# Kernel optimization log

Measured on AMD Instinct MI355X. Metric: run time of the kernel, lower is better.

The kernel has to match this reference:

```python
import jax, jax.numpy as jnp
import numpy as np

N_NODES = 50000
N_RAND_EDGES = 500000
SELF_LOOP_W = 0.5  # fill_value in add_remaining_self_loops


def _build_graph(key):
    k1, k2, k3 = jax.random.split(key, 3)
    src = jax.random.randint(k1, (N_RAND_EDGES,), 0, N_NODES)
    dst = jax.random.randint(k2, (N_RAND_EDGES,), 0, N_NODES)
    # PPMI weights are positive log-ratios; simulate with positive uniforms
    w = jax.random.uniform(k3, (N_RAND_EDGES,), minval=0.1, maxval=2.0)
    loops = jnp.arange(N_NODES)
    row = jnp.concatenate([src, loops])
    col = jnp.concatenate([dst, loops])
    ew = jnp.concatenate([w, jnp.full((N_NODES,), SELF_LOOP_W, dtype=w.dtype)])
    # symmetric normalization: D^-1/2 A D^-1/2 (deg computed from row, as in norm())
    deg = jax.ops.segment_sum(ew, row, num_segments=N_NODES)
    dis = jnp.where(deg > 0, deg ** -0.5, 0.0)
    norm = (dis[row] * ew * dis[col]).astype(jnp.float32)
    edge_index = jnp.stack([row, col]).astype(jnp.int64)
    return edge_index, norm


def setup_inputs() -> dict:
    key = jax.random.key(0)
    kx, kg, kw1, kw2 = jax.random.split(key, 4)
    edge_index, norm = _build_graph(kg)
    feat, hid, emb = 256, 128, 64
    # glorot init
    s1 = np.sqrt(6.0 / (feat + hid))
    s2 = np.sqrt(6.0 / (hid + emb))
    return {
        "x": jax.random.normal(kx, (N_NODES, feat), dtype=jnp.float32),
        "edge_index": edge_index,
        "norm": norm,
        "W1": jax.random.uniform(kw1, (feat, hid), minval=-s1, maxval=s1, dtype=jnp.float32),
        "b1": jnp.zeros((hid,), dtype=jnp.float32),
        "W2": jax.random.uniform(kw2, (hid, emb), minval=-s2, maxval=s2, dtype=jnp.float32),
        "b2": jnp.zeros((emb,), dtype=jnp.float32),
    }


def _gcn_layer(x, row, col, norm, W, b):
    h = x @ W                                   # [N, out]
    msg = norm[:, None] * h[row]                # gather + scale per edge
    agg = jax.ops.segment_sum(msg, col, num_segments=N_NODES)  # scatter-add
    return agg + b


def reference(x, edge_index, norm, W1, b1, W2, b2):
    row, col = edge_index[0], edge_index[1]
    h = _gcn_layer(x, row, col, norm, W1, b1)
    h = jax.nn.relu(h)  # dropout is identity in eval
    return _gcn_layer(h, row, col, norm, W2, b2)
```

## Files before the change

kernel.cpp:

```cpp
#include <hip/hip_runtime.h>
#include <stdint.h>


typedef __attribute__((ext_vector_type(8))) short short8;
typedef __attribute__((ext_vector_type(4))) float f32x4;

#define SLOTS 48
#define OCAP  65536

__device__ __forceinline__ unsigned short f2bf(float f) {
    unsigned u = __float_as_uint(f);
    return (unsigned short)((u + 0x7FFFu + ((u >> 16) & 1u)) >> 16);
}
__device__ __forceinline__ float bf_lo(unsigned v) { return __uint_as_float(v << 16); }
__device__ __forceinline__ float bf_hi(unsigned v) { return __uint_as_float(v & 0xFFFF0000u); }
__device__ __forceinline__ float bf1(unsigned short v) { return __uint_as_float((unsigned)v << 16); }
__device__ __forceinline__ unsigned short f2h(float f) {
    _Float16 h = (_Float16)f;
    return __builtin_bit_cast(unsigned short, h);
}
__device__ __forceinline__ float h2f(unsigned u16) {
    _Float16 h = __builtin_bit_cast(_Float16, (unsigned short)(u16 & 0xFFFFu));
    return (float)h;
}

__global__ __launch_bounds__(256) void k_prep0(int* __restrict__ cursor, int n,
                                               int* __restrict__ ocount,
                                               const float* __restrict__ W1,
                                               const float* __restrict__ W2,
                                               unsigned short* __restrict__ W1t,
                                               unsigned short* __restrict__ W2t,
                                               int FEAT, int HID, int EMB) {
    const int gid = blockIdx.x * blockDim.x + threadIdx.x;
    const int stride = gridDim.x * blockDim.x;
    if (gid == 0) *ocount = 0;
    int4* c4 = (int4*)cursor;
    const int n4 = n >> 2;
    for (int j = gid; j < n4; j += stride) c4[j] = make_int4(0, 0, 0, 0);
    for (int j = (n4 << 2) + gid; j < n; j += stride) cursor[j] = 0;
    const int t1 = FEAT * HID, t2 = HID * EMB;
    for (int i = gid; i < t1 + t2; i += stride) {
        if (i < t1) {
            int k = i / HID, nn = i % HID;
            W1t[(size_t)nn * FEAT + k] = f2bf(W1[i]);
        } else {
            int j = i - t1;
            int k = j / EMB, nn = j % EMB;
            W2t[(size_t)nn * HID + k] = f2bf(W2[j]);
        }
    }
}

template <int BM, int BN, int FM, int FN, bool A_F32, bool OUT_BF16>
__device__ __forceinline__ void gemm_body(char* ldsA, char* ldsB,
                                          const void* __restrict__ Ag,
                                          const unsigned short* __restrict__ Bt,
                                          void* __restrict__ Cv,
                                          int M, int K, int N, int blk) {
    const int tid  = threadIdx.x;
    const int lane = tid & 63;
    const int wid  = tid >> 6;
    const int wr   = wid >> 1;
    const int wc   = wid & 1;
    const int m0   = blk * BM;

    f32x4 acc[FM][FN] = {};

    for (int k0 = 0; k0 < K; k0 += 64) {
        {
            const int row  = tid >> 2;
            const int kq   = tid & 3;
            const int grow = min(m0 + row, M - 1);
            const int kbb  = kq * 32;
            const int sw   = (row & 7) << 4;
            if (A_F32) {
                const float* src = (const float*)Ag + (size_t)grow * K + k0 + kq * 16;
                float4 v0 = ((const float4*)src)[0];
                float4 v1 = ((const float4*)src)[1];
                float4 v2 = ((const float4*)src)[2];
                float4 v3 = ((const float4*)src)[3];
                union { short8 s; unsigned short h[8]; } p0, p1;
                p0.h[0] = f2bf(v0.x); p0.h[1] = f2bf(v0.y);
                p0.h[2] = f2bf(v0.z); p0.h[3] = f2bf(v0.w);
                p0.h[4] = f2bf(v1.x); p0.h[5] = f2bf(v1.y);
                p0.h[6] = f2bf(v1.z); p0.h[7] = f2bf(v1.w);
                p1.h[0] = f2bf(v2.x); p1.h[1] = f2bf(v2.y);
                p1.h[2] = f2bf(v2.z); p1.h[3] = f2bf(v2.w);
                p1.h[4] = f2bf(v3.x); p1.h[5] = f2bf(v3.y);
                p1.h[6] = f2bf(v3.z); p1.h[7] = f2bf(v3.w);
                *(short8*)(ldsA + row * 128 + ( kbb       ^ sw)) = p0.s;
                *(short8*)(ldsA + row * 128 + ((kbb + 16) ^ sw)) = p1.s;
            } else {
                const unsigned short* src =
                    (const unsigned short*)Ag + (size_t)grow * K + k0 + kq * 16;
                short8 s0 = ((const short8*)src)[0];
                short8 s1 = ((const short8*)src)[1];
                *(short8*)(ldsA + row * 128 + ( kbb       ^ sw)) = s0;
                *(short8*)(ldsA + row * 128 + ((kbb + 16) ^ sw)) = s1;
            }
        }
        if (BN == 128 || tid < 128) {
            const int row = tid >> 1;
            const int kh  = tid & 1;
            const int sw  = (row & 7) << 4;
            const short8* src = (const short8*)(Bt + (size_t)row * K + k0 + kh * 32);
            #pragma unroll
            for (int j = 0; j < 4; ++j) {
                short8 s = src[j];
                int kb = kh * 64 + j * 16;
                *(short8*)(ldsB + row * 128 + (kb ^ sw)) = s;
            }
        }
        __syncthreads();

        #pragma unroll
        for (int s = 0; s < 2; ++s) {
            const int klo = s * 64 + (lane >> 4) * 16;
            short8 af[FM], bfv[FN];
            #pragma unroll
            for (int i = 0; i < FM; ++i) {
                int r = wr * (FM * 16) + i * 16 + (lane & 15);
                af[i] = *(const short8*)(ldsA + r * 128 + (klo ^ ((r & 7) << 4)));
            }
            #pragma unroll
            for (int j = 0; j < FN; ++j) {
                int n = wc * (FN * 16) + j * 16 + (lane & 15);
                bfv[j] = *(const short8*)(ldsB + n * 128 + (klo ^ ((n & 7) << 4)));
            }
            #pragma unroll
            for (int i = 0; i < FM; ++i)
                #pragma unroll
                for (int j = 0; j < FN; ++j)
                    acc[i][j] = __builtin_amdgcn_mfma_f32_16x16x32_bf16(
                        af[i], bfv[j], acc[i][j], 0, 0, 0);
        }
        __syncthreads();
    }

    #pragma unroll
    for (int i = 0; i < FM; ++i) {
        const int rbase = m0 + wr * (FM * 16) + i * 16 + ((lane >> 4) << 2);
        #pragma unroll
        for (int j = 0; j < FN; ++j) {
            const int c = wc * (FN * 16) + j * 16 + (lane & 15);
            #pragma unroll
            for (int r = 0; r < 4; ++r)
                if (rbase + r < M) {
                    if (OUT_BF16)
                        ((unsigned short*)Cv)[(size_t)(rbase + r) * N + c] = f2bf(acc[i][j][r]);
                    else
                        ((float*)Cv)[(size_t)(rbase + r) * N + c] = acc[i][j][r];
                }
        }
    }
}

template <int BM, int BN, int FM, int FN, bool A_F32, bool OUT_BF16>
__global__ __launch_bounds__(256) void k_gemm_mfma(const void* __restrict__ Ag,
                                                   const unsigned short* __restrict__ Bt,
                                                   void* __restrict__ Cv,
                                                   int M, int K, int N) {
    __shared__ char ldsA[BM * 128];
    __shared__ char ldsB[BN * 128];
    gemm_body<BM, BN, FM, FN, A_F32, OUT_BF16>(ldsA, ldsB, Ag, Bt, Cv, M, K, N,
                                               blockIdx.x);
}

template <int BM, int BN, int FM, int FN, bool A_F32, bool OUT_BF16>
__global__ __launch_bounds__(256) void k_gemm_scatter(const void* __restrict__ Ag,
                                                      const unsigned short* __restrict__ Bt,
                                                      void* __restrict__ Cv,
                                                      int M, int K, int N,
                                                      int gemmBlocks,
                                                      const int* __restrict__ ei,
                                                      const float* __restrict__ nrm,
                                                      int E, int Nn,
                                                      int* __restrict__ cursor,
                                                      unsigned* __restrict__ ent,
                                                      uint2* __restrict__ olist,
                                                      int* __restrict__ ocount) {
    __shared__ char ldsA[BM * 128];
    __shared__ char ldsB[BN * 128];
    if ((int)blockIdx.x < gemmBlocks) {
        gemm_body<BM, BN, FM, FN, A_F32, OUT_BF16>(ldsA, ldsB, Ag, Bt, Cv, M, K, N,
                                                   blockIdx.x);
        return;
    }
    __shared__ int sIs64;
    if (threadIdx.x < 64) {
        const int i = 1 + 2 * threadIdx.x;
        int z = (i < 2 * E) ? (ei[i] == 0) : 1;
        unsigned long long m = __ballot(z);
        if (threadIdx.x == 0) sIs64 = (m == ~0ULL) ? 1 : 0;
    }
    __syncthreads();
    const int is64 = sIs64;

    const int t  = (blockIdx.x - gemmBlocks) * blockDim.x + threadIdx.x;
    const int e0 = t * 4;
    if (e0 >= E) return;

    int r[4], c[4];
    float wv[4];
    int nv = 4;
    if (e0 + 3 < E) {
        if (is64) {
            const int4* pr = (const int4*)(ei + 2 * e0);
            const int4* pc = (const int4*)(ei + 2 * E + 2 * e0);
            int4 r01 = pr[0], r23 = pr[1], c01 = pc[0], c23 = pc[1];
            r[0] = r01.x; r[1] = r01.z; r[2] = r23.x; r[3] = r23.z;
            c[0] = c01.x; c[1] = c01.z; c[2] = c23.x; c[3] = c23.z;
        } else {
            int4 rr = *(const int4*)(ei + e0);
            int4 cc = *(const int4*)(ei + E + e0);
            r[0] = rr.x; r[1] = rr.y; r[2] = rr.z; r[3] = rr.w;
            c[0] = cc.x; c[1] = cc.y; c[2] = cc.z; c[3] = cc.w;
        }
        const float4 w4 = *(const float4*)(nrm + e0);
        wv[0] = w4.x; wv[1] = w4.y; wv[2] = w4.z; wv[3] = w4.w;
    } else {
        nv = E - e0;
        for (int i = 0; i < nv; ++i) {
            const int e = e0 + i;
            if (is64) { r[i] = ei[2 * e]; c[i] = ei[2 * (E + e)]; }
            else      { r[i] = ei[e];     c[i] = ei[E + e]; }
            wv[i] = nrm[e];
        }
    }
    #pragma unroll
    for (int i = 0; i < 4; ++i) {
        if (i < nv && (unsigned)c[i] < (unsigned)Nn && (unsigned)r[i] < (unsigned)Nn) {
            const unsigned entry = ((unsigned)r[i] << 16) | (unsigned)f2h(wv[i]);
            const int pos = atomicAdd(&cursor[c[i]], 1);
            if (pos < SLOTS) ent[(size_t)c[i] * SLOTS + pos] = entry;
            else { int op = atomicAdd(ocount, 1);
                   if (op < OCAP) olist[op] = make_uint2((unsigned)c[i], entry); }
        }
    }
}

template <int F, bool RELU, bool OUT_BF16>
__global__ __launch_bounds__(256) void k_agg(const unsigned short* __restrict__ h,
                                             const int* __restrict__ cursor,
                                             const unsigned* __restrict__ ent,
                                             const uint2* __restrict__ olist,
                                             const int* __restrict__ ocount,
                                             const float* __restrict__ bias,
                                             void* __restrict__ outp, int nnodes) {
    const int lane = threadIdx.x & 63;
    const int wid  = __builtin_amdgcn_readfirstlane(threadIdx.x >> 6);
    const int node = blockIdx.x * 4 + wid;
    if (node >= nnodes) return;
    const int deg = min(cursor[node], SLOTS);
    const unsigned* slots = ent + (size_t)node * SLOTS;
    const unsigned rmax = (unsigned)(nnodes - 1);

    if (F == 128) {
        const unsigned* hp = (const unsigned*)h;
        float2 a0 = {0.f, 0.f}, a1 = {0.f, 0.f}, a2 = {0.f, 0.f}, a3 = {0.f, 0.f};
        for (int g = 0; g < deg; g += 4) {
            uint4 q = *(const uint4*)(slots + g);
            const int rem = deg - g;
            float w0 = h2f(q.x), w1 = h2f(q.y), w2 = h2f(q.z), w3 = h2f(q.w);
            if (rem < 4) {
                w1 = (rem > 1) ? w1 : 0.f;
                w2 = (rem > 2) ? w2 : 0.f;
                w3 = 0.f;
                if (rem == 3) w3 = 0.f; else if (rem > 3) {}
            }
            const unsigned v0 = hp[(size_t)min(q.x >> 16, rmax) * 64 + lane];
            const unsigned v1 = hp[(size_t)min(q.y >> 16, rmax) * 64 + lane];
            const unsigned v2 = hp[(size_t)min(q.z >> 16, rmax) * 64 + lane];
            const unsigned v3 = hp[(size_t)min(q.w >> 16, rmax) * 64 + lane];
            a0.x = fmaf(w0, bf_lo(v0), a0.x); a0.y = fmaf(w0, bf_hi(v0), a0.y);
            a1.x = fmaf(w1, bf_lo(v1), a1.x); a1.y = fmaf(w1, bf_hi(v1), a1.y);
            a2.x = fmaf(w2, bf_lo(v2), a2.x); a2.y = fmaf(w2, bf_hi(v2), a2.y);
            a3.x = fmaf(w3, bf_lo(v3), a3.x); a3.y = fmaf(w3, bf_hi(v3), a3.y);
        }
        float2 acc;
        acc.x = (a0.x + a1.x) + (a2.x + a3.x);
        acc.y = (a0.y + a1.y) + (a2.y + a3.y);
        const int oc = *ocount;
        if (oc > 0) {
            for (int i = 0; i < oc && i < OCAP; ++i) {
                const uint2 it = olist[i];
                if ((int)it.x == node) {
                    const float w = h2f(it.y);
                    const unsigned v = hp[(size_t)min(it.y >> 16, rmax) * 64 + lane];
                    acc.x = fmaf(w, bf_lo(v), acc.x);
                    acc.y = fmaf(w, bf_hi(v), acc.y);
                }
            }
        }
        const float2 b = ((const float2*)bias)[lane];
        acc.x += b.x; acc.y += b.y;
        if (RELU) { acc.x = fmaxf(acc.x, 0.f); acc.y = fmaxf(acc.y, 0.f); }
        if (OUT_BF16) {
            unsigned pack = (unsigned)f2bf(acc.x) | ((unsigned)f2bf(acc.y) << 16);
            ((unsigned*)outp)[(size_t)node * 64 + lane] = pack;
        } else {
            ((float2*)outp)[(size_t)node * 64 + lane] = acc;
        }
    } else {
        float a0 = 0.f, a1 = 0.f, a2 = 0.f, a3 = 0.f;
        for (int g = 0; g < deg; g += 4) {
            uint4 q = *(const uint4*)(slots + g);
            const int rem = deg - g;
            float w0 = h2f(q.x), w1 = h2f(q.y), w2 = h2f(q.z), w3 = h2f(q.w);
            if (rem < 4) {
                w1 = (rem > 1) ? w1 : 0.f;
                w2 = (rem > 2) ? w2 : 0.f;
                w3 = 0.f;
            }
            const float f0 = bf1(h[(size_t)min(q.x >> 16, rmax) * 64 + lane]);
            const float f1 = bf1(h[(size_t)min(q.y >> 16, rmax) * 64 + lane]);
            const float f2 = bf1(h[(size_t)min(q.z >> 16, rmax) * 64 + lane]);
            const float f3 = bf1(h[(size_t)min(q.w >> 16, rmax) * 64 + lane]);
            a0 = fmaf(w0, f0, a0); a1 = fmaf(w1, f1, a1);
            a2 = fmaf(w2, f2, a2); a3 = fmaf(w3, f3, a3);
        }
        float acc = (a0 + a1) + (a2 + a3);
        const int oc = *ocount;
        if (oc > 0) {
            for (int i = 0; i < oc && i < OCAP; ++i) {
                const uint2 it = olist[i];
                if ((int)it.x == node)
                    acc = fmaf(h2f(it.y),
                               bf1(h[(size_t)min(it.y >> 16, rmax) * 64 + lane]), acc);
            }
        }
        acc += bias[lane];
        if (RELU) acc = fmaxf(acc, 0.f);
        ((float*)outp)[(size_t)node * 64 + lane] = acc;
    }
}


extern "C" void kernel_launch(void* const* d_in, const int* in_sizes, int n_in,
                              void* d_out, int out_size, void* d_ws, size_t ws_size,
                              hipStream_t stream) {
    const float* x   = (const float*)d_in[0];
    const int*   ei  = (const int*)d_in[1];
    const float* nrm = (const float*)d_in[2];
    const float* W1  = (const float*)d_in[3];
    const float* b1  = (const float*)d_in[4];
    const float* W2  = (const float*)d_in[5];
    const float* b2  = (const float*)d_in[6];
    float* out = (float*)d_out;

    const int HID  = in_sizes[4];
    const int FEAT = in_sizes[3] / HID;
    const int EMB  = in_sizes[5] / HID;
    const int Nn   = in_sizes[0] / FEAT;
    const int E    = in_sizes[2];
    const int entWords = Nn * SLOTS;

    char* p = (char*)d_ws;
    auto alloc = [&](size_t bytes) {
        char* r = p;
        p += (bytes + 255) & ~(size_t)255;
        return r;
    };
    unsigned short* h1b    = (unsigned short*)alloc((size_t)Nn * HID * 2);
    unsigned short* a1b    = (unsigned short*)alloc((size_t)Nn * HID * 2);
    unsigned short* h2b    = (unsigned short*)alloc((size_t)Nn * EMB * 2);
    unsigned short* W1t    = (unsigned short*)alloc((size_t)HID * FEAT * 2);
    unsigned short* W2t    = (unsigned short*)alloc((size_t)EMB * HID * 2);
    int*            cursor = (int*)           alloc((size_t)Nn * 4);
    unsigned*       ent    = (unsigned*)      alloc((size_t)entWords * 4 + 256);
    uint2*          olist  = (uint2*)         alloc((size_t)OCAP * 8);
    int*            ocount = (int*)           alloc(256);

    const int sctBlocks  = (E + 4 * 256 - 1) / (4 * 256);
    const int gemmBlocks = (Nn + 63) / 64;

    k_prep0<<<128, 256, 0, stream>>>(cursor, Nn, ocount,
                                     W1, W2, W1t, W2t, FEAT, HID, EMB);
    k_gemm_scatter<64, 128, 2, 4, true, true>
        <<<gemmBlocks + sctBlocks, 256, 0, stream>>>(
            (const void*)x, W1t, (void*)h1b, Nn, FEAT, HID,
            gemmBlocks, ei, nrm, E, Nn, cursor, ent, olist, ocount);

    k_agg<128, true, true><<<(Nn + 3) / 4, 256, 0, stream>>>(
        h1b, cursor, ent, olist, ocount, b1, (void*)a1b, Nn);

    k_gemm_mfma<64, 64, 2, 2, false, true><<<gemmBlocks, 256, 0, stream>>>(
        (const void*)a1b, W2t, (void*)h2b, Nn, HID, EMB);
    k_agg<64, false, false><<<(Nn + 3) / 4, 256, 0, stream>>>(
        h2b, cursor, ent, olist, ocount, b2, (void*)out, Nn);
}
```

Baseline: 102.2 us.

## Pack edges in prep kernel and partition scatter by destination range

The prep kernel now reads edge_index and norm once and packs each edge into a compact 8-byte record (row<<16|col, fp16 weight). The fused GEMM+scatter kernel then reads these packed records, and each slice of edges is processed by 8 blocks, each handling only destinations in one eighth of the node range. The aim is to localize atomics and slot writes to a smaller address window for better cache behaviour. In exchange, every packed record is read 8 times, an extra record buffer is written, and the prep grid grows from 128 to 1024 blocks.

New measurement: 92.46 us, median of 2. 9.5% less time.

```diff
diff --git a/kernel.cpp b/kernel.cpp
--- a/kernel.cpp
+++ b/kernel.cpp
@@ -26,18 +26,34 @@
 
 __global__ __launch_bounds__(256) void k_prep0(int* __restrict__ cursor, int n,
                                                int* __restrict__ ocount,
+                                               const int* __restrict__ ei,
+                                               const float* __restrict__ nrm,
+                                               int E,
+                                               unsigned* __restrict__ rec,
                                                const float* __restrict__ W1,
                                                const float* __restrict__ W2,
                                                unsigned short* __restrict__ W1t,
                                                unsigned short* __restrict__ W2t,
                                                int FEAT, int HID, int EMB) {
+    __shared__ int sIs64;
+    if (threadIdx.x < 64) {
+        const int i = 1 + 2 * threadIdx.x;
+        int z = (i < 2 * E) ? (ei[i] == 0) : 1;
+        unsigned long long m = __ballot(z);
+        if (threadIdx.x == 0) sIs64 = (m == ~0ULL) ? 1 : 0;
+    }
+    __syncthreads();
+    const int is64 = sIs64;
+
     const int gid = blockIdx.x * blockDim.x + threadIdx.x;
     const int stride = gridDim.x * blockDim.x;
     if (gid == 0) *ocount = 0;
+
     int4* c4 = (int4*)cursor;
     const int n4 = n >> 2;
     for (int j = gid; j < n4; j += stride) c4[j] = make_int4(0, 0, 0, 0);
     for (int j = (n4 << 2) + gid; j < n; j += stride) cursor[j] = 0;
+
     const int t1 = FEAT * HID, t2 = HID * EMB;
     for (int i = gid; i < t1 + t2; i += stride) {
         if (i < t1) {
@@ -47,6 +63,58 @@
             int j = i - t1;
             int k = j / EMB, nn = j % EMB;
             W2t[(size_t)nn * HID + k] = f2bf(W2[j]);
+        }
+    }
+
+    const int nG = (E + 3) / 4;
+    for (int g = gid; g < nG; g += stride) {
+        const int e0 = g * 4;
+        if (e0 + 3 < E) {
+            int r[4], c[4];
+            if (is64) {
+                const int4* pr = (const int4*)(ei + 2 * e0);
+                const int4* pc = (const int4*)(ei + 2 * E + 2 * e0);
+                int4 r01 = pr[0], r23 = pr[1], c01 = pc[0], c23 = pc[1];
+                r[0] = r01.x; r[1] = r01.z; r[2] = r23.x; r[3] = r23.z;
+                c[0] = c01.x; c[1] = c01.z; c[2] = c23.x; c[3] = c23.z;
+            } else {
+                int4 rr = *(const int4*)(ei + e0);
+                int4 cc = *(const int4*)(ei + E + e0);
+                r[0] = rr.x; r[1] = rr.y; r[2] = rr.z; r[3] = rr.w;
+                c[0] = cc.x; c[1] = cc.y; c[2] = cc.z; c[3] = cc.w;
+            }
+            const float4 w4 = *(const float4*)(nrm + e0);
+            const float wv[4] = {w4.x, w4.y, w4.z, w4.w};
+            unsigned ow[8];
+            #pragma unroll
+            for (int i = 0; i < 4; ++i) {
+                unsigned a = 0xFFFFFFFFu, b = 0u;
+                if ((unsigned)c[i] < (unsigned)n && (unsigned)r[i] < (unsigned)n) {
+                    a = ((unsigned)r[i] << 16) | (unsigned)c[i];
+                    b = (unsigned)f2h(wv[i]);
+                }
+                ow[2 * i + 0] = a;
+                ow[2 * i + 1] = b;
+            }
+            uint4* dst = (uint4*)(rec + 2 * (size_t)e0);
+            dst[0] = make_uint4(ow[0], ow[1], ow[2], ow[3]);
+            dst[1] = make_uint4(ow[4], ow[5], ow[6], ow[7]);
+        } else {
+            for (int i = 0; i < 4; ++i) {
+                const int e = e0 + i;
+                unsigned a = 0xFFFFFFFFu, b = 0u;
+                if (e < E) {
+                    int rr, cc;
+                    if (is64) { rr = ei[2 * e]; cc = ei[2 * (E + e)]; }
+                    else      { rr = ei[e];     cc = ei[E + e]; }
+                    if ((unsigned)cc < (unsigned)n && (unsigned)rr < (unsigned)n) {
+                        a = ((unsigned)rr << 16) | (unsigned)cc;
+                        b = (unsigned)f2h(nrm[e]);
+                    }
+                }
+                rec[2 * (size_t)e + 0] = a;
+                rec[2 * (size_t)e + 1] = b;
+            }
         }
     }
 }
@@ -166,15 +234,14 @@
                                                blockIdx.x);
 }
 
-template <int BM, int BN, int FM, int FN, bool A_F32, bool OUT_BF16>
+template <int BM, int BN, int FM, int FN, bool A_F32, bool OUT_BF16, int PAIRS>
 __global__ __launch_bounds__(256) void k_gemm_scatter(const void* __restrict__ Ag,
                                                       const unsigned short* __restrict__ Bt,
                                                       void* __restrict__ Cv,
                                                       int M, int K, int N,
                                                       int gemmBlocks,
-                                                      const int* __restrict__ ei,
-                                                      const float* __restrict__ nrm,
-                                                      int E, int Nn,
+                                                      const uint4* __restrict__ rec4,
+                                                      int nPairs, int Nn,
                                                       int* __restrict__ cursor,
                                                       unsigned* __restrict__ ent,
                                                       uint2* __restrict__ olist,
@@ -186,55 +253,38 @@
                                                    blockIdx.x);
         return;
     }
-    __shared__ int sIs64;
-    if (threadIdx.x < 64) {
-        const int i = 1 + 2 * threadIdx.x;
-        int z = (i < 2 * E) ? (ei[i] == 0) : 1;
-        unsigned long long m = __ballot(z);
-        if (threadIdx.x == 0) sIs64 = (m == ~0ULL) ? 1 : 0;
-    }
-    __syncthreads();
-    const int is64 = sIs64;
-
-    const int t  = (blockIdx.x - gemmBlocks) * blockDim.x + threadIdx.x;
-    const int e0 = t * 4;
-    if (e0 >= E) return;
-
-    int r[4], c[4];
-    float wv[4];
-    int nv = 4;
-    if (e0 + 3 < E) {
-        if (is64) {
-            const int4* pr = (const int4*)(ei + 2 * e0);
-            const int4* pc = (const int4*)(ei + 2 * E + 2 * e0);
-            int4 r01 = pr[0], r23 = pr[1], c01 = pc[0], c23 = pc[1];
-            r[0] = r01.x; r[1] = r01.z; r[2] = r23.x; r[3] = r23.z;
-            c[0] = c01.x; c[1] = c01.z; c[2] = c23.x; c[3] = c23.z;
-        } else {
-            int4 rr = *(const int4*)(ei + e0);
-            int4 cc = *(const int4*)(ei + E + e0);
-            r[0] = rr.x; r[1] = rr.y; r[2] = rr.z; r[3] = rr.w;
-            c[0] = cc.x; c[1] = cc.y; c[2] = cc.z; c[3] = cc.w;
-        }
-        const float4 w4 = *(const float4*)(nrm + e0);
-        wv[0] = w4.x; wv[1] = w4.y; wv[2] = w4.z; wv[3] = w4.w;
-    } else {
-        nv = E - e0;
-        for (int i = 0; i < nv; ++i) {
-            const int e = e0 + i;
-            if (is64) { r[i] = ei[2 * e]; c[i] = ei[2 * (E + e)]; }
-            else      { r[i] = ei[e];     c[i] = ei[E + e]; }
-            wv[i] = nrm[e];
-        }
-    }
+    const int part  = blockIdx.x & 7;
+    const int slice = (blockIdx.x - gemmBlocks) >> 3;
+    const int np    = (Nn + 7) / 8;
+    const unsigned lo = (unsigned)(part * np);
+    const unsigned hi = (unsigned)min(Nn, (int)lo + np);
+
+    const int base = slice * (256 * PAIRS) + threadIdx.x;
     #pragma unroll
-    for (int i = 0; i < 4; ++i) {
-        if (i < nv && (unsigned)c[i] < (unsigned)Nn && (unsigned)r[i] < (unsigned)Nn) {
-            const unsigned entry = ((unsigned)r[i] << 16) | (unsigned)f2h(wv[i]);
-            const int pos = atomicAdd(&cursor[c[i]], 1);
-            if (pos < SLOTS) ent[(size_t)c[i] * SLOTS + pos] = entry;
-            else { int op = atomicAdd(ocount, 1);
-                   if (op < OCAP) olist[op] = make_uint2((unsigned)c[i], entry); }
+    for (int j = 0; j < PAIRS; ++j) {
+        const int p = base + j * 256;
+        if (p < nPairs) {
+            const uint4 q = rec4[p];
+            if (q.x != 0xFFFFFFFFu) {
+                const unsigned d = q.x & 0xFFFFu;
+                if (d >= lo && d < hi) {
+                    const unsigned entry = (q.x & 0xFFFF0000u) | q.y;
+                    const int pos = atomicAdd(&cursor[d], 1);
+                    if (pos < SLOTS) ent[(size_t)d * SLOTS + pos] = entry;
+                    else { int op = atomicAdd(ocount, 1);
+                           if (op < OCAP) olist[op] = make_uint2(d, entry); }
+                }
+            }
+            if (q.z != 0xFFFFFFFFu) {
+                const unsigned d = q.z & 0xFFFFu;
+                if (d >= lo && d < hi) {
+                    const unsigned entry = (q.z & 0xFFFF0000u) | q.w;
+                    const int pos = atomicAdd(&cursor[d], 1);
+                    if (pos < SLOTS) ent[(size_t)d * SLOTS + pos] = entry;
+                    else { int op = atomicAdd(ocount, 1);
+                           if (op < OCAP) olist[op] = make_uint2(d, entry); }
+                }
+            }
         }
     }
 }
@@ -266,7 +316,6 @@
                 w1 = (rem > 1) ? w1 : 0.f;
                 w2 = (rem > 2) ? w2 : 0.f;
                 w3 = 0.f;
-                if (rem == 3) w3 = 0.f; else if (rem > 3) {}
             }
             const unsigned v0 = hp[(size_t)min(q.x >> 16, rmax) * 64 + lane];
             const unsigned v1 = hp[(size_t)min(q.y >> 16, rmax) * 64 + lane];
@@ -353,6 +402,7 @@
     const int EMB  = in_sizes[5] / HID;
     const int Nn   = in_sizes[0] / FEAT;
     const int E    = in_sizes[2];
+    const int E4   = (E + 3) & ~3;
     const int entWords = Nn * SLOTS;
 
     char* p = (char*)d_ws;
@@ -368,18 +418,22 @@
     unsigned short* W2t    = (unsigned short*)alloc((size_t)EMB * HID * 2);
     int*            cursor = (int*)           alloc((size_t)Nn * 4);
     unsigned*       ent    = (unsigned*)      alloc((size_t)entWords * 4 + 256);
+    unsigned*       rec    = (unsigned*)      alloc((size_t)E4 * 8);
     uint2*          olist  = (uint2*)         alloc((size_t)OCAP * 8);
     int*            ocount = (int*)           alloc(256);
 
-    const int sctBlocks  = (E + 4 * 256 - 1) / (4 * 256);
+    constexpr int PAIRS  = 2;
+    const int nPairs     = E4 / 2;
+    const int sctSlices  = (nPairs + 256 * PAIRS - 1) / (256 * PAIRS);
+    const int sctBlocks  = sctSlices * 8;
     const int gemmBlocks = (Nn + 63) / 64;
 
-    k_prep0<<<128, 256, 0, stream>>>(cursor, Nn, ocount,
-                                     W1, W2, W1t, W2t, FEAT, HID, EMB);
-    k_gemm_scatter<64, 128, 2, 4, true, true>
+    k_prep0<<<1024, 256, 0, stream>>>(cursor, Nn, ocount, ei, nrm, E, rec,
+                                      W1, W2, W1t, W2t, FEAT, HID, EMB);
+    k_gemm_scatter<64, 128, 2, 4, true, true, PAIRS>
         <<<gemmBlocks + sctBlocks, 256, 0, stream>>>(
             (const void*)x, W1t, (void*)h1b, Nn, FEAT, HID,
-            gemmBlocks, ei, nrm, E, Nn, cursor, ent, olist, ocount);
+            gemmBlocks, (const uint4*)rec, nPairs, Nn, cursor, ent, olist, ocount);
 
     k_agg<128, true, true><<<(Nn + 3) / 4, 256, 0, stream>>>(
         h1b, cursor, ent, olist, ocount, b1, (void*)a1b, Nn);
```

## Pre-bucket edges by destination range so scatter atomics stay XCD-local

Applied to the files above, without the earlier changes.

Adds a bucketing kernel that splits edges into 8 buckets by destination-node range. It uses block-local LDS counters and one global atomic per bucket per block, and it also takes over the weight transposes. The scatter blocks inside the fused GEMM kernel now read one bucket chosen by blockIdx&7, so all cursor and slot atomics for a node range come from the same XCD's blocks and L2. This removes cross-die contention on the atomics, at the cost of an extra launch and an extra write and read of the edge list through the bucket buffer. Edges that overflow a bucket's capacity fall back to the direct slot-append path.

Result: no change. 100.9 us (-1.3%).

```diff
diff --git a/kernel.cpp b/kernel.cpp
--- a/kernel.cpp
+++ b/kernel.cpp
@@ -24,20 +24,60 @@
     return (float)h;
 }
 
-__global__ __launch_bounds__(256) void k_prep0(int* __restrict__ cursor, int n,
-                                               int* __restrict__ ocount,
-                                               const float* __restrict__ W1,
-                                               const float* __restrict__ W2,
-                                               unsigned short* __restrict__ W1t,
-                                               unsigned short* __restrict__ W2t,
-                                               int FEAT, int HID, int EMB) {
+__device__ __forceinline__ void slot_append(unsigned d, unsigned entry,
+                                            int* __restrict__ cursor,
+                                            unsigned* __restrict__ ent,
+                                            uint2* __restrict__ olist,
+                                            int* __restrict__ ocount) {
+    const int pos = atomicAdd(&cursor[d], 1);
+    if (pos < SLOTS) ent[(size_t)d * SLOTS + pos] = entry;
+    else {
+        int op = atomicAdd(ocount, 1);
+        if (op < OCAP) olist[op] = make_uint2(d, entry);
+    }
+}
+
+__global__ __launch_bounds__(256) void k_prep_z(int* __restrict__ cursor, int n,
+                                                int* __restrict__ bCnt,
+                                                int* __restrict__ ocount) {
     const int gid = blockIdx.x * blockDim.x + threadIdx.x;
     const int stride = gridDim.x * blockDim.x;
     if (gid == 0) *ocount = 0;
+    if (gid < 8) bCnt[gid] = 0;
     int4* c4 = (int4*)cursor;
     const int n4 = n >> 2;
     for (int j = gid; j < n4; j += stride) c4[j] = make_int4(0, 0, 0, 0);
     for (int j = (n4 << 2) + gid; j < n; j += stride) cursor[j] = 0;
+}
+
+__global__ __launch_bounds__(256) void k_bucket(const int* __restrict__ ei,
+                                                const float* __restrict__ nrm,
+                                                int E, int Nn,
+                                                uint2* __restrict__ bucket, int CAP,
+                                                int* __restrict__ bCnt,
+                                                int* __restrict__ cursor,
+                                                unsigned* __restrict__ ent,
+                                                uint2* __restrict__ olist,
+                                                int* __restrict__ ocount,
+                                                const float* __restrict__ W1,
+                                                const float* __restrict__ W2,
+                                                unsigned short* __restrict__ W1t,
+                                                unsigned short* __restrict__ W2t,
+                                                int FEAT, int HID, int EMB) {
+    __shared__ int sIs64;
+    __shared__ int lCnt[8], lBase[8];
+    if (threadIdx.x < 64) {
+        const int i = 1 + 2 * threadIdx.x;
+        int z = (i < 2 * E) ? (ei[i] == 0) : 1;
+        unsigned long long m = __ballot(z);
+        if (threadIdx.x == 0) sIs64 = (m == ~0ULL) ? 1 : 0;
+    }
+    __syncthreads();
+    const int is64 = sIs64;
+
+    const int gid = blockIdx.x * blockDim.x + threadIdx.x;
+    const int stride = gridDim.x * blockDim.x;
+
     const int t1 = FEAT * HID, t2 = HID * EMB;
     for (int i = gid; i < t1 + t2; i += stride) {
         if (i < t1) {
@@ -48,6 +88,83 @@
             int k = j / EMB, nn = j % EMB;
             W2t[(size_t)nn * HID + k] = f2bf(W2[j]);
         }
+    }
+
+    const int np = (Nn + 7) / 8;
+    const int nG = (E + 3) / 4;
+    const int nRounds = (nG + stride - 1) / stride;
+
+    for (int rd = 0; rd < nRounds; ++rd) {
+        const int g = rd * stride + gid;
+        int valid[4] = {0, 0, 0, 0};
+        unsigned a[4];
+        unsigned w16[4];
+        int bkt[4], rank[4];
+
+        if (g < nG) {
+            const int e0 = g * 4;
+            int r[4], c[4];
+            float wv[4];
+            int nv = 4;
+            if (e0 + 3 < E) {
+                if (is64) {
+                    const int4* pr = (const int4*)(ei + 2 * e0);
+                    const int4* pc = (const int4*)(ei + 2 * E + 2 * e0);
+                    int4 r01 = pr[0], r23 = pr[1], c01 = pc[0], c23 = pc[1];
+                    r[0] = r01.x; r[1] = r01.z; r[2] = r23.x; r[3] = r23.z;
+                    c[0] = c01.x; c[1] = c01.z; c[2] = c23.x; c[3] = c23.z;
+                } else {
+                    int4 rr = *(const int4*)(ei + e0);
+                    int4 cc = *(const int4*)(ei + E + e0);
+                    r[0] = rr.x; r[1] = rr.y; r[2] = rr.z; r[3] = rr.w;
+                    c[0] = cc.x; c[1] = cc.y; c[2] = cc.z; c[3] = cc.w;
+                }
+                const float4 w4 = *(const float4*)(nrm + e0);
+                wv[0] = w4.x; wv[1] = w4.y; wv[2] = w4.z; wv[3] = w4.w;
+            } else {
+                nv = E - e0;
+                for (int i = 0; i < nv; ++i) {
+                    const int e = e0 + i;
+                    if (is64) { r[i] = ei[2 * e]; c[i] = ei[2 * (E + e)]; }
+                    else      { r[i] = ei[e];     c[i] = ei[E + e]; }
+                    wv[i] = nrm[e];
+                }
+            }
+            #pragma unroll
+            for (int i = 0; i < 4; ++i) {
+                if (i < nv && (unsigned)c[i] < (unsigned)Nn &&
+                    (unsigned)r[i] < (unsigned)Nn) {
+                    valid[i] = 1;
+                    a[i]   = ((unsigned)r[i] << 16) | (unsigned)c[i];
+                    w16[i] = (unsigned)f2h(wv[i]);
+                    bkt[i] = c[i] / np;
+                }
+            }
+        }
+
+        if (threadIdx.x < 8) lCnt[threadIdx.x] = 0;
+        __syncthreads();
+        #pragma unroll
+        for (int i = 0; i < 4; ++i)
+            if (valid[i]) rank[i] = atomicAdd(&lCnt[bkt[i]], 1);
+        __syncthreads();
+        if (threadIdx.x < 8) {
+            const int cnt = lCnt[threadIdx.x];
+            lBase[threadIdx.x] = (cnt > 0) ? atomicAdd(&bCnt[threadIdx.x], cnt) : 0;
+        }
+        __syncthreads();
+        #pragma unroll
+        for (int i = 0; i < 4; ++i) {
+            if (valid[i]) {
+                const int gpos = lBase[bkt[i]] + rank[i];
+                if (gpos < CAP)
+                    bucket[(size_t)bkt[i] * CAP + gpos] = make_uint2(a[i], w16[i]);
+                else
+                    slot_append(a[i] & 0xFFFFu, (a[i] & 0xFFFF0000u) | w16[i],
+                                cursor, ent, olist, ocount);
+            }
+        }
+        __syncthreads();
     }
 }
 
@@ -166,15 +283,15 @@
                                                blockIdx.x);
 }
 
-template <int BM, int BN, int FM, int FN, bool A_F32, bool OUT_BF16>
+template <int BM, int BN, int FM, int FN, bool A_F32, bool OUT_BF16, int EPT>
 __global__ __launch_bounds__(256) void k_gemm_scatter(const void* __restrict__ Ag,
                                                       const unsigned short* __restrict__ Bt,
                                                       void* __restrict__ Cv,
                                                       int M, int K, int N,
                                                       int gemmBlocks,
-                                                      const int* __restrict__ ei,
-                                                      const float* __restrict__ nrm,
-                                                      int E, int Nn,
+                                                      const uint2* __restrict__ bucket,
+                                                      int CAP,
+                                                      const int* __restrict__ bCnt,
                                                       int* __restrict__ cursor,
                                                       unsigned* __restrict__ ent,
                                                       uint2* __restrict__ olist,
@@ -186,55 +303,18 @@
                                                    blockIdx.x);
         return;
     }
-    __shared__ int sIs64;
-    if (threadIdx.x < 64) {
-        const int i = 1 + 2 * threadIdx.x;
-        int z = (i < 2 * E) ? (ei[i] == 0) : 1;
-        unsigned long long m = __ballot(z);
-        if (threadIdx.x == 0) sIs64 = (m == ~0ULL) ? 1 : 0;
-    }
-    __syncthreads();
-    const int is64 = sIs64;
-
-    const int t  = (blockIdx.x - gemmBlocks) * blockDim.x + threadIdx.x;
-    const int e0 = t * 4;
-    if (e0 >= E) return;
-
-    int r[4], c[4];
-    float wv[4];
-    int nv = 4;
-    if (e0 + 3 < E) {
-        if (is64) {
-            const int4* pr = (const int4*)(ei + 2 * e0);
-            const int4* pc = (const int4*)(ei + 2 * E + 2 * e0);
-            int4 r01 = pr[0], r23 = pr[1], c01 = pc[0], c23 = pc[1];
-            r[0] = r01.x; r[1] = r01.z; r[2] = r23.x; r[3] = r23.z;
-            c[0] = c01.x; c[1] = c01.z; c[2] = c23.x; c[3] = c23.z;
-        } else {
-            int4 rr = *(const int4*)(ei + e0);
-            int4 cc = *(const int4*)(ei + E + e0);
-            r[0] = rr.x; r[1] = rr.y; r[2] = rr.z; r[3] = rr.w;
-            c[0] = cc.x; c[1] = cc.y; c[2] = cc.z; c[3] = cc.w;
-        }
-        const float4 w4 = *(const float4*)(nrm + e0);
-        wv[0] = w4.x; wv[1] = w4.y; wv[2] = w4.z; wv[3] = w4.w;
-    } else {
-        nv = E - e0;
-        for (int i = 0; i < nv; ++i) {
-            const int e = e0 + i;
-            if (is64) { r[i] = ei[2 * e]; c[i] = ei[2 * (E + e)]; }
-            else      { r[i] = ei[e];     c[i] = ei[E + e]; }
-            wv[i] = nrm[e];
-        }
-    }
+    const int part  = blockIdx.x & 7;
+    const int slice = (blockIdx.x - gemmBlocks) >> 3;
+    const int n = min(bCnt[part], CAP);
+    const uint2* bk = bucket + (size_t)part * CAP;
+
     #pragma unroll
-    for (int i = 0; i < 4; ++i) {
-        if (i < nv && (unsigned)c[i] < (unsigned)Nn && (unsigned)r[i] < (unsigned)Nn) {
-            const unsigned entry = ((unsigned)r[i] << 16) | (unsigned)f2h(wv[i]);
-            const int pos = atomicAdd(&cursor[c[i]], 1);
-            if (pos < SLOTS) ent[(size_t)c[i] * SLOTS + pos] = entry;
-            else { int op = atomicAdd(ocount, 1);
-                   if (op < OCAP) olist[op] = make_uint2((unsigned)c[i], entry); }
+    for (int j = 0; j < EPT; ++j) {
+        const int idx = slice * (256 * EPT) + j * 256 + threadIdx.x;
+        if (idx < n) {
+            const uint2 q = bk[idx];
+            slot_append(q.x & 0xFFFFu, (q.x & 0xFFFF0000u) | q.y,
+                        cursor, ent, olist, ocount);
         }
     }
 }
@@ -266,7 +346,6 @@
                 w1 = (rem > 1) ? w1 : 0.f;
                 w2 = (rem > 2) ? w2 : 0.f;
                 w3 = 0.f;
-                if (rem == 3) w3 = 0.f; else if (rem > 3) {}
             }
             const unsigned v0 = hp[(size_t)min(q.x >> 16, rmax) * 64 + lane];
             const unsigned v1 = hp[(size_t)min(q.y >> 16, rmax) * 64 + lane];
@@ -353,6 +432,7 @@
     const int EMB  = in_sizes[5] / HID;
     const int Nn   = in_sizes[0] / FEAT;
     const int E    = in_sizes[2];
+    const int CAP  = (E + 3) / 4;
     const int entWords = Nn * SLOTS;
 
     char* p = (char*)d_ws;
@@ -368,18 +448,24 @@
     unsigned short* W2t    = (unsigned short*)alloc((size_t)EMB * HID * 2);
     int*            cursor = (int*)           alloc((size_t)Nn * 4);
     unsigned*       ent    = (unsigned*)      alloc((size_t)entWords * 4 + 256);
+    uint2*          bucket = (uint2*)         alloc((size_t)8 * CAP * 8);
+    int*            bCnt   = (int*)           alloc(256);
     uint2*          olist  = (uint2*)         alloc((size_t)OCAP * 8);
     int*            ocount = (int*)           alloc(256);
 
-    const int sctBlocks  = (E + 4 * 256 - 1) / (4 * 256);
+    constexpr int EPT = 4;
+    const int sctSlices  = (CAP + 256 * EPT - 1) / (256 * EPT);
+    const int sctBlocks  = sctSlices * 8;
     const int gemmBlocks = (Nn + 63) / 64;
 
-    k_prep0<<<128, 256, 0, stream>>>(cursor, Nn, ocount,
-                                     W1, W2, W1t, W2t, FEAT, HID, EMB);
-    k_gemm_scatter<64, 128, 2, 4, true, true>
+    k_prep_z<<<128, 256, 0, stream>>>(cursor, Nn, bCnt, ocount);
+    k_bucket<<<1024, 256, 0, stream>>>(ei, nrm, E, Nn, bucket, CAP, bCnt,
+                                       cursor, ent, olist, ocount,
+                                       W1, W2, W1t, W2t, FEAT, HID, EMB);
+    k_gemm_scatter<64, 128, 2, 4, true, true, EPT>
         <<<gemmBlocks + sctBlocks, 256, 0, stream>>>(
             (const void*)x, W1t, (void*)h1b, Nn, FEAT, HID,
-            gemmBlocks, ei, nrm, E, Nn, cursor, ent, olist, ocount);
+            gemmBlocks, bucket, CAP, bCnt, cursor, ent, olist, ocount);
 
     k_agg<128, true, true><<<(Nn + 3) / 4, 256, 0, stream>>>(
         h1b, cursor, ent, olist, ocount, b1, (void*)a1b, Nn);
```
